# Kernel tuning notes

Hardware: AMD Instinct MI355X
Metric: run time of the kernel (lower is better)

Reference implementation:

```python
import jax, jax.numpy as jnp
import numpy as np
import math

B, T, E, D = 4, 2048, 1024, 4

def _tau_init(t):
    a = 0.1 ** (1.0 / max(t - 1, 1))
    tt = -math.log(max(a, 1e-10))
    return math.log(math.exp(tt) - 1 + 1e-10)

def causal_ema(b, tau_raw):
    # h_t = alpha * h_{t-1} + b_t with alpha = exp(-softplus(tau_raw));
    # exactly equal to the conv1d with kernel exp(-tau*j) in the original.
    alpha = jnp.exp(-jax.nn.softplus(tau_raw)).astype(b.dtype)
    def step(h, bt):
        h = alpha * h + bt
        return h, h
    h0 = jnp.zeros((b.shape[0], b.shape[2]), b.dtype)
    _, hs = jax.lax.scan(step, h0, jnp.swapaxes(b, 0, 1))  # scan over T
    return jnp.swapaxes(hs, 0, 1)

def setup_inputs():
    key = jax.random.key(0)
    ks = jax.random.split(key, 10)
    s = 0.02
    return {
        "x": jax.random.normal(ks[0], (B, T, E), jnp.float32),
        "tau_ctx": jnp.float32(_tau_init(max(T // 2, 4))),
        "tau_raws": jnp.array([_tau_init(max(T // 2 ** i, 2)) for i in range(D)], jnp.float32),
        "Wg": jax.random.normal(ks[1], (E, 2 * E), jnp.float32) * s,
        "bg": jnp.full((E,), -0.5, jnp.float32),
        "Wn1": jax.random.normal(ks[2], (E // 4, E), jnp.float32) * s,
        "bn1": jnp.zeros((E // 4,), jnp.float32),
        "Wn2": jax.random.normal(ks[3], (D, E // 4), jnp.float32) * s,
        "bn2": jnp.zeros((D,), jnp.float32),
        "blend": jax.random.normal(ks[4], (D, E), jnp.float32) * s,
        "Wsoma": jax.random.normal(ks[5], (E, E), jnp.float32) * s,
        "bsoma": jnp.zeros((E,), jnp.float32),
        "Wtemp": jax.random.normal(ks[6], (E, E), jnp.float32) * s,
        "btemp": jnp.zeros((E,), jnp.float32),
        "Wout": jax.random.normal(ks[7], (E, E), jnp.float32) * s,
        "gamma": jnp.ones((E,), jnp.float32),
        "beta": jnp.zeros((E,), jnp.float32),
    }

def reference(x, tau_ctx, tau_raws, Wg, bg, Wn1, bn1, Wn2, bn2, blend, Wsoma, bsoma, Wtemp, btemp, Wout, gamma, beta):
    ctx = causal_ema(x, tau_ctx)                                   # (B,T,E)
    gate_in = jnp.concatenate([x, ctx], axis=-1)                   # (B,T,2E)
    wg = jax.nn.sigmoid(jnp.einsum('btc,ec->bte', gate_in, Wg) + bg)
    gated = x * wg
    h1 = jax.nn.gelu(jnp.einsum('btc,hc->bth', x, Wn1) + bn1, approximate=False)
    mod = 0.5 + jax.nn.sigmoid(jnp.einsum('bth,dh->btd', h1, Wn2) + bn2)  # (B,T,D)
    # neuromod_ema: modulate input then fixed-alpha EMA, one per dendrite
    traces = jax.vmap(lambda tau, m: causal_ema(gated * m[..., None], tau))(
        tau_raws, jnp.moveaxis(mod, -1, 0))                        # (D,B,T,E)
    blend_w = jax.nn.softmax(blend, axis=0)                        # (D,E)
    temporal = jnp.einsum('dbtc,dc->btc', traces, blend_w)
    gate = jax.nn.sigmoid(jnp.einsum('btc,ec->bte', temporal, Wtemp) + btemp)
    soma = jax.nn.gelu(jnp.einsum('btc,ec->bte', x, Wsoma) + bsoma, approximate=False)
    out = jnp.einsum('btc,ec->bte', soma * gate, Wout)
    mu = out.mean(-1, keepdims=True)
    var = out.var(-1, keepdims=True)
    return (out - mu) / jnp.sqrt(var + 1e-5) * gamma + beta
```

## Files before the change

### kernel.cpp

```cpp
#include <hip/hip_runtime.h>
#include <math.h>

#define B_DIM 4
#define T_DIM 2048
#define E_DIM 1024
#define M_ROWS (B_DIM*T_DIM)
#define NC 32
#define CL (T_DIM/NC)

typedef short short8 __attribute__((ext_vector_type(8)));
typedef float f32x4 __attribute__((ext_vector_type(4)));

__device__ __forceinline__ float bf2f(unsigned short u){
  union { unsigned int i; float f; } c; c.i = ((unsigned int)u) << 16; return c.f;
}
__device__ __forceinline__ unsigned short f2bf(float f){
  union { float f; unsigned int i; } c; c.f = f;
  unsigned int u = c.i;
  return (unsigned short)((u + 0x7FFFu + ((u >> 16) & 1u)) >> 16);
}
__device__ __forceinline__ unsigned int pack2(float a, float b){
  return (unsigned int)f2bf(a) | ((unsigned int)f2bf(b) << 16);
}
__device__ __forceinline__ float sigf(float x){ return 1.f/(1.f+__expf(-x)); }
__device__ __forceinline__ float geluf(float x){ return 0.5f*x*(1.f+erff(x*0.70710678118f)); }

__device__ __forceinline__ void glds16(const unsigned short* g, unsigned short* l){
  __builtin_amdgcn_global_load_lds((const __attribute__((address_space(1))) void*)g,
                                   (__attribute__((address_space(3))) void*)l, 16, 0, 0);
}

__device__ __forceinline__ void cvt4(const float* __restrict__ s, unsigned short* __restrict__ d){
  float4 v = *(const float4*)s;
  uint2 p; p.x = pack2(v.x, v.y); p.y = pack2(v.z, v.w);
  *(uint2*)d = p;
}

__global__ __launch_bounds__(256) void conv_all_k(
    const float* __restrict__ Wg, const float* __restrict__ Wsoma,
    const float* __restrict__ Wn1, const float* __restrict__ Wtemp,
    const float* __restrict__ Wout, const float* __restrict__ bsoma,
    const float* __restrict__ bn1,
    unsigned short* __restrict__ wg_bf, unsigned short* __restrict__ wsn1,
    unsigned short* __restrict__ wtemp_bf, unsigned short* __restrict__ wout_bf,
    float* __restrict__ bsn1){
  int u = blockIdx.x*256 + threadIdx.x;
  if (u < 524288){ cvt4(Wg + (size_t)u*4, wg_bf + (size_t)u*4); }
  else if (u < 786432){ u -= 524288; cvt4(Wsoma + (size_t)u*4, wsn1 + (size_t)u*4); }
  else if (u < 851968){ u -= 786432; cvt4(Wn1 + (size_t)u*4, wsn1 + 1048576 + (size_t)u*4); }
  else if (u < 1114112){ u -= 851968; cvt4(Wtemp + (size_t)u*4, wtemp_bf + (size_t)u*4); }
  else if (u < 1376256){ u -= 1114112; cvt4(Wout + (size_t)u*4, wout_bf + (size_t)u*4); }
  else if (u < 1376576){
    u -= 1376256; int i = u*4;
    float4 v = (i < 1024) ? *(const float4*)&bsoma[i] : *(const float4*)&bn1[i-1024];
    *(float4*)&bsn1[i] = v;
  }
}

__global__ __launch_bounds__(256) void ctx_carry_k(const float* __restrict__ x,
                                                   const float* __restrict__ tau_ctx,
                                                   float* __restrict__ car){
  int gid = blockIdx.x*256 + threadIdx.x;
  int e2 = (gid & 511)*2, bc = gid >> 9;
  int b = bc >> 5, chunk = bc & 31;
  float alpha = 1.f/(1.f+expf(tau_ctx[0]));
  const float2* xp = (const float2*)(x + ((size_t)b*T_DIM + chunk*CL)*E_DIM + e2);
  float h0 = 0.f, h1 = 0.f;
  #pragma unroll 8
  for (int t = 0; t < CL; t++){
    float2 v = xp[(size_t)t*512];
    h0 = alpha*h0 + v.x; h1 = alpha*h1 + v.y;
  }
  *(float2*)&car[(size_t)bc*E_DIM + e2] = make_float2(h0, h1);
}

__global__ __launch_bounds__(256) void ctx_scan_k(const float* __restrict__ x,
                                                  const float* __restrict__ tau_ctx,
                                                  const float* __restrict__ car,
                                                  unsigned short* __restrict__ gatein){
  int gid = blockIdx.x*256 + threadIdx.x;
  int e2 = (gid & 511)*2, bc = gid >> 9;
  int b = bc >> 5, chunk = bc & 31;
  float alpha = 1.f/(1.f+expf(tau_ctx[0]));
  float alphaL = powf(alpha, (float)CL);
  float h0 = 0.f, h1 = 0.f;
  for (int j = 0; j < chunk; j++){
    float2 c = *(const float2*)&car[(size_t)(b*NC + j)*E_DIM + e2];
    h0 = alphaL*h0 + c.x; h1 = alphaL*h1 + c.y;
  }
  const float2* xp = (const float2*)(x + ((size_t)b*T_DIM + chunk*CL)*E_DIM + e2);
  unsigned int* op = (unsigned int*)(gatein + ((size_t)(b*T_DIM + chunk*CL))*2048 + e2);
  #pragma unroll 4
  for (int t = 0; t < CL; t++){
    float2 v = xp[(size_t)t*512];
    h0 = alpha*h0 + v.x; h1 = alpha*h1 + v.y;
    op[(size_t)t*1024]       = pack2(v.x, v.y);
    op[(size_t)t*1024 + 512] = pack2(h0, h1);
  }
}

__global__ __launch_bounds__(256) void dend_carry_k(const unsigned short* __restrict__ gated,
                                                    const float* __restrict__ mod,
                                                    const float* __restrict__ tau_raws,
                                                    float* __restrict__ car){
  int gid = blockIdx.x*256 + threadIdx.x;
  int e2 = (gid & 511)*2, bc = gid >> 9;
  int b = bc >> 5, chunk = bc & 31;
  float a[4];
  #pragma unroll
  for (int d = 0; d < 4; d++) a[d] = 1.f/(1.f+expf(tau_raws[d]));
  const ushort2* gp = (const ushort2*)(gated + ((size_t)(b*T_DIM + chunk*CL))*E_DIM + e2);
  const float4* mp = (const float4*)(mod + (size_t)(b*T_DIM + chunk*CL)*4);
  float hx[4] = {0,0,0,0}, hy[4] = {0,0,0,0};
  #pragma unroll 4
  for (int t = 0; t < CL; t++){
    ushort2 gv = gp[(size_t)t*512];
    float gx = bf2f(gv.x), gy = bf2f(gv.y);
    float4 m4 = mp[t];
    hx[0] = a[0]*hx[0] + gx*m4.x; hy[0] = a[0]*hy[0] + gy*m4.x;
    hx[1] = a[1]*hx[1] + gx*m4.y; hy[1] = a[1]*hy[1] + gy*m4.y;
    hx[2] = a[2]*hx[2] + gx*m4.z; hy[2] = a[2]*hy[2] + gy*m4.z;
    hx[3] = a[3]*hx[3] + gx*m4.w; hy[3] = a[3]*hy[3] + gy*m4.w;
  }
  #pragma unroll
  for (int d = 0; d < 4; d++)
    *(float2*)&car[(size_t)d*131072 + (size_t)bc*E_DIM + e2] = make_float2(hx[d], hy[d]);
}

__global__ __launch_bounds__(256) void dend_scan_k(const unsigned short* __restrict__ gated,
                                                   const float* __restrict__ mod,
                                                   const float* __restrict__ tau_raws,
                                                   const float* __restrict__ car,
                                                   const float* __restrict__ blend,
                                                   unsigned short* __restrict__ temporal){
  int gid = blockIdx.x*256 + threadIdx.x;
  int e2 = (gid & 511)*2, bc = gid >> 9;
  int b = bc >> 5, chunk = bc & 31;
  float a[4], hx[4], hy[4];
  #pragma unroll
  for (int d = 0; d < 4; d++) a[d] = 1.f/(1.f+expf(tau_raws[d]));
  #pragma unroll
  for (int d = 0; d < 4; d++){
    float aL = powf(a[d], (float)CL);
    float h0 = 0.f, h1 = 0.f;
    for (int j = 0; j < chunk; j++){
      float2 c = *(const float2*)&car[(size_t)d*131072 + (size_t)(b*NC + j)*E_DIM + e2];
      h0 = aL*h0 + c.x; h1 = aL*h1 + c.y;
    }
    hx[d] = h0; hy[d] = h1;
  }
  float blx[4], bly[4];
  #pragma unroll
  for (int d = 0; d < 4; d++){
    float2 bl = *(const float2*)&blend[(size_t)d*E_DIM + e2];
    blx[d] = bl.x; bly[d] = bl.y;
  }
  float mxx = fmaxf(fmaxf(blx[0],blx[1]), fmaxf(blx[2],blx[3]));
  float mxy = fmaxf(fmaxf(bly[0],bly[1]), fmaxf(bly[2],bly[3]));
  float wx[4], wy[4], sx = 0.f, sy = 0.f;
  #pragma unroll
  for (int d = 0; d < 4; d++){ wx[d] = __expf(blx[d]-mxx); sx += wx[d];
                               wy[d] = __expf(bly[d]-mxy); sy += wy[d]; }
  float ix = 1.f/sx, iy = 1.f/sy;
  #pragma unroll
  for (int d = 0; d < 4; d++){ wx[d] *= ix; wy[d] *= iy; }

  const ushort2* gp = (const ushort2*)(gated + ((size_t)(b*T_DIM + chunk*CL))*E_DIM + e2);
  const float4* mp = (const float4*)(mod + (size_t)(b*T_DIM + chunk*CL)*4);
  unsigned int* op = (unsigned int*)(temporal + ((size_t)(b*T_DIM + chunk*CL))*E_DIM + e2);
  #pragma unroll 4
  for (int t = 0; t < CL; t++){
    ushort2 gv = gp[(size_t)t*512];
    float gx = bf2f(gv.x), gy = bf2f(gv.y);
    float4 m4 = mp[t];
    hx[0] = a[0]*hx[0] + gx*m4.x; hy[0] = a[0]*hy[0] + gy*m4.x;
    hx[1] = a[1]*hx[1] + gx*m4.y; hy[1] = a[1]*hy[1] + gy*m4.y;
    hx[2] = a[2]*hx[2] + gx*m4.z; hy[2] = a[2]*hy[2] + gy*m4.z;
    hx[3] = a[3]*hx[3] + gx*m4.w; hy[3] = a[3]*hy[3] + gy*m4.w;
    float tvx = wx[0]*hx[0] + wx[1]*hx[1] + wx[2]*hx[2] + wx[3]*hx[3];
    float tvy = wy[0]*hy[0] + wy[1]*hy[1] + wy[2]*hy[2] + wy[3]*hy[3];
    op[(size_t)t*512] = pack2(tvx, tvy);
  }
}

__global__ __launch_bounds__(256) void mod_k(const unsigned short* __restrict__ h1,
                                             const float* __restrict__ Wn2,
                                             const float* __restrict__ bn2,
                                             float* __restrict__ mod){
  int wave = threadIdx.x >> 6, lane = threadIdx.x & 63;
  int m = blockIdx.x*4 + wave;
  float p0=0.f,p1=0.f,p2=0.f,p3=0.f;
  for (int c = lane; c < 256; c += 64){
    float h = bf2f(h1[(size_t)m*256 + c]);
    p0 += h*Wn2[0*256 + c]; p1 += h*Wn2[1*256 + c];
    p2 += h*Wn2[2*256 + c]; p3 += h*Wn2[3*256 + c];
  }
  #pragma unroll
  for (int off = 32; off > 0; off >>= 1){
    p0 += __shfl_down(p0, off); p1 += __shfl_down(p1, off);
    p2 += __shfl_down(p2, off); p3 += __shfl_down(p3, off);
  }
  if (lane == 0){
    mod[(size_t)m*4 + 0] = 0.5f + sigf(p0 + bn2[0]);
    mod[(size_t)m*4 + 1] = 0.5f + sigf(p1 + bn2[1]);
    mod[(size_t)m*4 + 2] = 0.5f + sigf(p2 + bn2[2]);
    mod[(size_t)m*4 + 3] = 0.5f + sigf(p3 + bn2[3]);
  }
}

template<int EPI>
__global__ __launch_bounds__(256, 2) void gemm_k(
    const unsigned short* __restrict__ A, int lda,
    const unsigned short* __restrict__ Bw, int K,
    const float* __restrict__ bias,
    const float* __restrict__ xf32,
    const unsigned short* __restrict__ ebf,
    void* __restrict__ outp, void* __restrict__ outp2)
{
  __shared__ unsigned short sA[128*32];
  __shared__ unsigned short sB[128*32];
  const int tid = threadIdx.x;
  const int wv = tid >> 6, lane = tid & 63;
  const int quad = lane >> 4, l15 = lane & 15;
  const int wm = (wv & 1) * 64, wn = (wv >> 1) * 64;
  const int row0 = blockIdx.x * 128, col0 = blockIdx.y * 128;

  const int r = tid >> 2, kc = (tid & 3) * 8;
  const unsigned short* pa0 = A  + (size_t)(row0 + r)*lda      + kc;
  const unsigned short* pa1 = A  + (size_t)(row0 + 64 + r)*lda + kc;
  const unsigned short* pb0 = Bw + (size_t)(col0 + r)*K        + kc;
  const unsigned short* pb1 = Bw + (size_t)(col0 + 64 + r)*K   + kc;
  unsigned short* la0 = &sA[wv*512];
  unsigned short* la1 = &sA[2048 + wv*512];
  unsigned short* lb0 = &sB[wv*512];
  unsigned short* lb1 = &sB[2048 + wv*512];

  f32x4 acc[4][4];
  #pragma unroll
  for (int i = 0; i < 4; i++)
    #pragma unroll
    for (int j = 0; j < 4; j++) acc[i][j] = (f32x4){0.f,0.f,0.f,0.f};

  for (int k0 = 0; k0 < K; k0 += 32){
    __syncthreads();
    glds16(pa0 + k0, la0);
    glds16(pa1 + k0, la1);
    glds16(pb0 + k0, lb0);
    glds16(pb1 + k0, lb1);
    __syncthreads();
    short8 afr[4], bfr[4];
    #pragma unroll
    for (int i = 0; i < 4; i++) afr[i] = *(const short8*)&sA[(wm + i*16 + l15)*32 + quad*8];
    #pragma unroll
    for (int j = 0; j < 4; j++) bfr[j] = *(const short8*)&sB[(wn + j*16 + l15)*32 + quad*8];
    #pragma unroll
    for (int i = 0; i < 4; i++)
      #pragma unroll
      for (int j = 0; j < 4; j++)
        acc[i][j] = __builtin_amdgcn_mfma_f32_16x16x32_bf16(afr[i], bfr[j], acc[i][j], 0, 0, 0);
  }

  #pragma unroll
  for (int i = 0; i < 4; i++){
    #pragma unroll
    for (int j = 0; j < 4; j++){
      const int col = col0 + wn + j*16 + l15;
      #pragma unroll
      for (int rr = 0; rr < 4; rr++){
        const int row = row0 + wm + i*16 + quad*4 + rr;
        float v = acc[i][j][rr];
        if (EPI == 0){
          size_t o = (size_t)row*1024 + col;
          v += bias[col];
          ((unsigned short*)outp)[o] = f2bf(xf32[o] * sigf(v));
        } else if (EPI == 1){
          v += bias[col];
          float g = geluf(v);
          if (col < 1024) ((unsigned short*)outp )[(size_t)row*1024 + col]        = f2bf(g);
          else            ((unsigned short*)outp2)[(size_t)row*256  + (col-1024)] = f2bf(g);
        } else if (EPI == 2){
          size_t o = (size_t)row*1024 + col;
          v += bias[col];
          ((unsigned short*)outp)[o] = f2bf(sigf(v) * bf2f(ebf[o]));
        } else {
          ((float*)outp)[(size_t)row*1024 + col] = v;
        }
      }
    }
  }
}

__global__ __launch_bounds__(256) void ln_k(const float* __restrict__ in,
                                            const float* __restrict__ gamma,
                                            const float* __restrict__ beta,
                                            float* __restrict__ out){
  __shared__ float s1[4], s2[4];
  int row = blockIdx.x, tid = threadIdx.x;
  float4 v = *(const float4*)&in[(size_t)row*1024 + tid*4];
  float s = v.x+v.y+v.z+v.w;
  float q = v.x*v.x+v.y*v.y+v.z*v.z+v.w*v.w;
  #pragma unroll
  for (int off = 32; off > 0; off >>= 1){ s += __shfl_down(s, off); q += __shfl_down(q, off); }
  int wave = tid >> 6, lane = tid & 63;
  if (lane == 0){ s1[wave] = s; s2[wave] = q; }
  __syncthreads();
  s = s1[0]+s1[1]+s1[2]+s1[3];
  q = s2[0]+s2[1]+s2[2]+s2[3];
  float mu = s*(1.f/1024.f);
  float var = q*(1.f/1024.f) - mu*mu;
  float rs = rsqrtf(var + 1e-5f);
  int c = tid*4;
  float4 g = *(const float4*)&gamma[c];
  float4 bb = *(const float4*)&beta[c];
  float4 o;
  o.x = (v.x-mu)*rs*g.x + bb.x;
  o.y = (v.y-mu)*rs*g.y + bb.y;
  o.z = (v.z-mu)*rs*g.z + bb.z;
  o.w = (v.w-mu)*rs*g.w + bb.w;
  *(float4*)&out[(size_t)row*1024 + c] = o;
}

extern "C" void kernel_launch(void* const* d_in, const int* in_sizes, int n_in,
                              void* d_out, int out_size, void* d_ws, size_t ws_size,
                              hipStream_t stream) {
  const float* x        = (const float*)d_in[0];
  const float* tau_ctx  = (const float*)d_in[1];
  const float* tau_raws = (const float*)d_in[2];
  const float* Wg       = (const float*)d_in[3];
  const float* bg       = (const float*)d_in[4];
  const float* Wn1      = (const float*)d_in[5];
  const float* bn1      = (const float*)d_in[6];
  const float* Wn2      = (const float*)d_in[7];
  const float* bn2      = (const float*)d_in[8];
  const float* blend    = (const float*)d_in[9];
  const float* Wsoma    = (const float*)d_in[10];
  const float* bsoma    = (const float*)d_in[11];
  const float* Wtemp    = (const float*)d_in[12];
  const float* btemp    = (const float*)d_in[13];
  const float* Wout     = (const float*)d_in[14];
  const float* gamma    = (const float*)d_in[15];
  const float* beta     = (const float*)d_in[16];

  char* ws = (char*)d_ws;
  unsigned short* gatein   = (unsigned short*)(ws + 0);
  float*          out_pre  = (float*)(ws + 0);
  unsigned short* wg_bf    = (unsigned short*)(ws + 33554432);
  unsigned short* wsn1     = (unsigned short*)(ws + 37748736);
  unsigned short* wtemp_bf = (unsigned short*)(ws + 40370176);
  unsigned short* wout_bf  = (unsigned short*)(ws + 42467328);
  float*          bsn1     = (float*)(ws + 44564480);
  unsigned short* h1_bf    = (unsigned short*)(ws + 44572672);
  float*          car_d    = (float*)(ws + 44572672);
  float*          car_ctx  = (float*)(ws + 48766976);
  float*          modbuf   = (float*)(ws + 48766976);
  unsigned short* gated    = (unsigned short*)(ws + 49291264);
  unsigned short* sg       = gated;
  unsigned short* temporal = (unsigned short*)(ws + 66068480);
  unsigned short* soma     = (unsigned short*)(ws + 82845696);

  conv_all_k<<<dim3(5378), dim3(256), 0, stream>>>(Wg, Wsoma, Wn1, Wtemp, Wout, bsoma, bn1,
                                                   wg_bf, wsn1, wtemp_bf, wout_bf, bsn1);

  ctx_carry_k<<<dim3(256), dim3(256), 0, stream>>>(x, tau_ctx, car_ctx);
  ctx_scan_k <<<dim3(256), dim3(256), 0, stream>>>(x, tau_ctx, car_ctx, gatein);

  gemm_k<0><<<dim3(64, 8), dim3(256), 0, stream>>>(
      gatein, 2048, wg_bf, 2048, bg, x, nullptr, gated, nullptr);

  gemm_k<1><<<dim3(64, 10), dim3(256), 0, stream>>>(
      gatein, 2048, wsn1, 1024, bsn1, nullptr, nullptr, soma, h1_bf);

  mod_k<<<dim3(M_ROWS/4), dim3(256), 0, stream>>>(h1_bf, Wn2, bn2, modbuf);

  dend_carry_k<<<dim3(256), dim3(256), 0, stream>>>(gated, modbuf, tau_raws, car_d);
  dend_scan_k <<<dim3(256), dim3(256), 0, stream>>>(gated, modbuf, tau_raws, car_d, blend, temporal);

  gemm_k<2><<<dim3(64, 8), dim3(256), 0, stream>>>(
      temporal, 1024, wtemp_bf, 1024, btemp, nullptr, soma, sg, nullptr);

  gemm_k<3><<<dim3(64, 8), dim3(256), 0, stream>>>(
      sg, 1024, wout_bf, 1024, nullptr, nullptr, nullptr, out_pre, nullptr);

  ln_k<<<dim3(M_ROWS), dim3(256), 0, stream>>>(out_pre, gamma, beta, (float*)d_out);
}
```

Baseline: 387.0 us.

## Double-buffer GEMM LDS tiles and merge first two GEMMs into one launch

Adds double-buffered shared-memory staging to the GEMM kernels, so the global-to-LDS loads for the next K tile are issued while MFMAs run on the current one, and one barrier per iteration is dropped. The gate GEMM and the soma/neuron GEMM now run as a single 64x18-block launch whose blocks pick their weight matrix and epilogue by blockIdx.y. This removes a launch and lets both GEMMs fill the device together. The gated epilogue now reads x as bf16 from gatein instead of the fp32 x, which changes precision slightly. Doubling the LDS footprint may lower occupancy.

```diff
diff --git a/kernel.cpp b/kernel.cpp
--- a/kernel.cpp
+++ b/kernel.cpp
@@ -208,17 +208,128 @@
   }
 }
 
+__global__ __launch_bounds__(256, 2) void gemm1_k(
+    const unsigned short* __restrict__ gatein,
+    const unsigned short* __restrict__ wg_bf,
+    const unsigned short* __restrict__ wsn1,
+    const float* __restrict__ bg,
+    const float* __restrict__ bsn1,
+    unsigned short* __restrict__ gated,
+    unsigned short* __restrict__ soma,
+    unsigned short* __restrict__ h1)
+{
+  __shared__ unsigned short sA[2][4096];
+  __shared__ unsigned short sB[2][4096];
+  const int tid = threadIdx.x;
+  const int wv = tid >> 6, lane = tid & 63;
+  const int quad = lane >> 4, l15 = lane & 15;
+  const int wm = (wv & 1) * 64, wn = (wv >> 1) * 64;
+  const int row0 = blockIdx.x * 128;
+  const int by = blockIdx.y;
+
+  int mode, colw0, K;
+  const unsigned short* Bw;
+  const float* bias;
+  if (by < 8)       { mode = 0; colw0 = by*128;            Bw = wg_bf + (size_t)colw0*2048; K = 2048; bias = bg   + colw0; }
+  else if (by < 16) { mode = 1; colw0 = (by-8)*128;        Bw = wsn1  + (size_t)colw0*1024; K = 1024; bias = bsn1 + colw0; }
+  else              { mode = 2; colw0 = 1024 + (by-16)*128; Bw = wsn1 + (size_t)colw0*1024; K = 1024; bias = bsn1 + colw0; }
+
+  const int r = tid >> 2, kc = (tid & 3) * 8;
+  const unsigned short* pa0 = gatein + (size_t)(row0 + r)*2048      + kc;
+  const unsigned short* pa1 = gatein + (size_t)(row0 + 64 + r)*2048 + kc;
+  const unsigned short* pb0 = Bw + (size_t)r*K        + kc;
+  const unsigned short* pb1 = Bw + (size_t)(64 + r)*K + kc;
+
+  f32x4 acc[4][4];
+  #pragma unroll
+  for (int i = 0; i < 4; i++)
+    #pragma unroll
+    for (int j = 0; j < 4; j++) acc[i][j] = (f32x4){0.f,0.f,0.f,0.f};
+
+  glds16(pa0, &sA[0][wv*512]);
+  glds16(pa1, &sA[0][2048 + wv*512]);
+  glds16(pb0, &sB[0][wv*512]);
+  glds16(pb1, &sB[0][2048 + wv*512]);
+
+  const int nk = K >> 5;
+  for (int it = 0; it < nk; it++){
+    __syncthreads();
+    const int cur = it & 1, nxt = cur ^ 1;
+    if (it + 1 < nk){
+      const int ko = (it + 1) << 5;
+      glds16(pa0 + ko, &sA[nxt][wv*512]);
+      glds16(pa1 + ko, &sA[nxt][2048 + wv*512]);
+      glds16(pb0 + ko, &sB[nxt][wv*512]);
+      glds16(pb1 + ko, &sB[nxt][2048 + wv*512]);
+    }
+    short8 afr[4], bfr[4];
+    #pragma unroll
+    for (int i = 0; i < 4; i++) afr[i] = *(const short8*)&sA[cur][(wm + i*16 + l15)*32 + quad*8];
+    #pragma unroll
+    for (int j = 0; j < 4; j++) bfr[j] = *(const short8*)&sB[cur][(wn + j*16 + l15)*32 + quad*8];
+    #pragma unroll
+    for (int i = 0; i < 4; i++)
+      #pragma unroll
+      for (int j = 0; j < 4; j++)
+        acc[i][j] = __builtin_amdgcn_mfma_f32_16x16x32_bf16(afr[i], bfr[j], acc[i][j], 0, 0, 0);
+  }
+
+  if (mode == 0){
+    #pragma unroll
+    for (int i = 0; i < 4; i++)
+      #pragma unroll
+      for (int j = 0; j < 4; j++){
+        const int lc = wn + j*16 + l15;
+        const int col = colw0 + lc;
+        #pragma unroll
+        for (int rr = 0; rr < 4; rr++){
+          const int row = row0 + wm + i*16 + quad*4 + rr;
+          float v = acc[i][j][rr] + bias[lc];
+          float xv = bf2f(gatein[(size_t)row*2048 + col]);
+          gated[(size_t)row*1024 + col] = f2bf(xv * sigf(v));
+        }
+      }
+  } else if (mode == 1){
+    #pragma unroll
+    for (int i = 0; i < 4; i++)
+      #pragma unroll
+      for (int j = 0; j < 4; j++){
+        const int lc = wn + j*16 + l15;
+        const int col = colw0 + lc;
+        #pragma unroll
+        for (int rr = 0; rr < 4; rr++){
+          const int row = row0 + wm + i*16 + quad*4 + rr;
+          float v = acc[i][j][rr] + bias[lc];
+          soma[(size_t)row*1024 + col] = f2bf(geluf(v));
+        }
+      }
+  } else {
+    #pragma unroll
+    for (int i = 0; i < 4; i++)
+      #pragma unroll
+      for (int j = 0; j < 4; j++){
+        const int lc = wn + j*16 + l15;
+        const int col = colw0 - 1024 + lc;
+        #pragma unroll
+        for (int rr = 0; rr < 4; rr++){
+          const int row = row0 + wm + i*16 + quad*4 + rr;
+          float v = acc[i][j][rr] + bias[lc];
+          h1[(size_t)row*256 + col] = f2bf(geluf(v));
+        }
+      }
+  }
+}
+
 template<int EPI>
 __global__ __launch_bounds__(256, 2) void gemm_k(
-    const unsigned short* __restrict__ A, int lda,
-    const unsigned short* __restrict__ Bw, int K,
+    const unsigned short* __restrict__ A,
+    const unsigned short* __restrict__ Bw,
     const float* __restrict__ bias,
-    const float* __restrict__ xf32,
     const unsigned short* __restrict__ ebf,
-    void* __restrict__ outp, void* __restrict__ outp2)
+    void* __restrict__ outp)
 {
-  __shared__ unsigned short sA[128*32];
-  __shared__ unsigned short sB[128*32];
+  __shared__ unsigned short sA[2][4096];
+  __shared__ unsigned short sB[2][4096];
   const int tid = threadIdx.x;
   const int wv = tid >> 6, lane = tid & 63;
   const int quad = lane >> 4, l15 = lane & 15;
@@ -226,14 +337,10 @@
   const int row0 = blockIdx.x * 128, col0 = blockIdx.y * 128;
 
   const int r = tid >> 2, kc = (tid & 3) * 8;
-  const unsigned short* pa0 = A  + (size_t)(row0 + r)*lda      + kc;
-  const unsigned short* pa1 = A  + (size_t)(row0 + 64 + r)*lda + kc;
-  const unsigned short* pb0 = Bw + (size_t)(col0 + r)*K        + kc;
-  const unsigned short* pb1 = Bw + (size_t)(col0 + 64 + r)*K   + kc;
-  unsigned short* la0 = &sA[wv*512];
-  unsigned short* la1 = &sA[2048 + wv*512];
-  unsigned short* lb0 = &sB[wv*512];
-  unsigned short* lb1 = &sB[2048 + wv*512];
+  const unsigned short* pa0 = A  + (size_t)(row0 + r)*1024      + kc;
+  const unsigned short* pa1 = A  + (size_t)(row0 + 64 + r)*1024 + kc;
+  const unsigned short* pb0 = Bw + (size_t)(col0 + r)*1024      + kc;
+  const unsigned short* pb1 = Bw + (size_t)(col0 + 64 + r)*1024 + kc;
 
   f32x4 acc[4][4];
   #pragma unroll
@@ -241,18 +348,26 @@
     #pragma unroll
     for (int j = 0; j < 4; j++) acc[i][j] = (f32x4){0.f,0.f,0.f,0.f};
 
-  for (int k0 = 0; k0 < K; k0 += 32){
+  glds16(pa0, &sA[0][wv*512]);
+  glds16(pa1, &sA[0][2048 + wv*512]);
+  glds16(pb0, &sB[0][wv*512]);
+  glds16(pb1, &sB[0][2048 + wv*512]);
+
+  for (int it = 0; it < 32; it++){
     __syncthreads();
-    glds16(pa0 + k0, la0);
-    glds16(pa1 + k0, la1);
-    glds16(pb0 + k0, lb0);
-    glds16(pb1 + k0, lb1);
-    __syncthreads();
+    const int cur = it & 1, nxt = cur ^ 1;
+    if (it + 1 < 32){
+      const int ko = (it + 1) << 5;
+      glds16(pa0 + ko, &sA[nxt][wv*512]);
+      glds16(pa1 + ko, &sA[nxt][2048 + wv*512]);
+      glds16(pb0 + ko, &sB[nxt][wv*512]);
+      glds16(pb1 + ko, &sB[nxt][2048 + wv*512]);
+    }
     short8 afr[4], bfr[4];
     #pragma unroll
-    for (int i = 0; i < 4; i++) afr[i] = *(const short8*)&sA[(wm + i*16 + l15)*32 + quad*8];
-    #pragma unroll
-    for (int j = 0; j < 4; j++) bfr[j] = *(const short8*)&sB[(wn + j*16 + l15)*32 + quad*8];
+    for (int i = 0; i < 4; i++) afr[i] = *(const short8*)&sA[cur][(wm + i*16 + l15)*32 + quad*8];
+    #pragma unroll
+    for (int j = 0; j < 4; j++) bfr[j] = *(const short8*)&sB[cur][(wn + j*16 + l15)*32 + quad*8];
     #pragma unroll
     for (int i = 0; i < 4; i++)
       #pragma unroll
@@ -261,7 +376,7 @@
   }
 
   #pragma unroll
-  for (int i = 0; i < 4; i++){
+  for (int i = 0; i < 4; i++)
     #pragma unroll
     for (int j = 0; j < 4; j++){
       const int col = col0 + wn + j*16 + l15;
@@ -269,25 +384,15 @@
       for (int rr = 0; rr < 4; rr++){
         const int row = row0 + wm + i*16 + quad*4 + rr;
         float v = acc[i][j][rr];
-        if (EPI == 0){
-          size_t o = (size_t)row*1024 + col;
-          v += bias[col];
-          ((unsigned short*)outp)[o] = f2bf(xf32[o] * sigf(v));
-        } else if (EPI == 1){
-          v += bias[col];
-          float g = geluf(v);
-          if (col < 1024) ((unsigned short*)outp )[(size_t)row*1024 + col]        = f2bf(g);
-          else            ((unsigned short*)outp2)[(size_t)row*256  + (col-1024)] = f2bf(g);
-        } else if (EPI == 2){
-          size_t o = (size_t)row*1024 + col;
+        size_t o = (size_t)row*1024 + col;
+        if (EPI == 2){
           v += bias[col];
           ((unsigned short*)outp)[o] = f2bf(sigf(v) * bf2f(ebf[o]));
         } else {
-          ((float*)outp)[(size_t)row*1024 + col] = v;
+          ((float*)outp)[o] = v;
         }
       }
     }
-  }
 }
 
 __global__ __launch_bounds__(256) void ln_k(const float* __restrict__ in,
@@ -364,22 +469,17 @@
   ctx_carry_k<<<dim3(256), dim3(256), 0, stream>>>(x, tau_ctx, car_ctx);
   ctx_scan_k <<<dim3(256), dim3(256), 0, stream>>>(x, tau_ctx, car_ctx, gatein);
 
-  gemm_k<0><<<dim3(64, 8), dim3(256), 0, stream>>>(
-      gatein, 2048, wg_bf, 2048, bg, x, nullptr, gated, nullptr);
-
-  gemm_k<1><<<dim3(64, 10), dim3(256), 0, stream>>>(
-      gatein, 2048, wsn1, 1024, bsn1, nullptr, nullptr, soma, h1_bf);
+  gemm1_k<<<dim3(64, 18), dim3(256), 0, stream>>>(gatein, wg_bf, wsn1, bg, bsn1,
+                                                  gated, soma, h1_bf);
 
   mod_k<<<dim3(M_ROWS/4), dim3(256), 0, stream>>>(h1_bf, Wn2, bn2, modbuf);
 
   dend_carry_k<<<dim3(256), dim3(256), 0, stream>>>(gated, modbuf, tau_raws, car_d);
   dend_scan_k <<<dim3(256), dim3(256), 0, stream>>>(gated, modbuf, tau_raws, car_d, blend, temporal);
 
-  gemm_k<2><<<dim3(64, 8), dim3(256), 0, stream>>>(
-      temporal, 1024, wtemp_bf, 1024, btemp, nullptr, soma, sg, nullptr);
-
-  gemm_k<3><<<dim3(64, 8), dim3(256), 0, stream>>>(
-      sg, 1024, wout_bf, 1024, nullptr, nullptr, nullptr, out_pre, nullptr);
+  gemm_k<2><<<dim3(64, 8), dim3(256), 0, stream>>>(temporal, wtemp_bf, btemp, soma, sg);
+
+  gemm_k<3><<<dim3(64, 8), dim3(256), 0, stream>>>(sg, wout_bf, nullptr, nullptr, out_pre);
 
   ln_k<<<dim3(M_ROWS), dim3(256), 0, stream>>>(out_pre, gamma, beta, (float*)d_out);
 }
```

After: 342.8 us. 1.13x faster.
